# Kernel optimization log

Measured on AMD Instinct MI355X. Metric: run time of the kernel, lower is better.

## Reference

```python
import jax, jax.numpy as jnp
import numpy as np

N = 100000   # num variables
D_IN = 512
D_OUT = 512
C = 4096     # num clusters
K = 32       # vars per cluster
E = 16384    # cluster edges
S = 16       # shared vars per edge
H = 4        # num heads
NEG_SLOPE = 0.2


def setup_inputs() -> dict:
    key = jax.random.key(0)
    ks = jax.random.split(key, 8)
    xav = (6.0 / (D_IN + D_OUT)) ** 0.5  # xavier_uniform bound
    x_var = jax.random.normal(ks[0], (N, D_IN), dtype=jnp.float32)
    W_Q = jax.random.uniform(ks[1], (D_OUT, D_IN), jnp.float32, -xav, xav)
    W_K = jax.random.uniform(ks[2], (D_OUT, D_IN), jnp.float32, -xav, xav)
    W_V = jax.random.uniform(ks[3], (D_OUT, D_IN), jnp.float32, -xav, xav)
    head_weights = jnp.ones((H,), jnp.float32)
    cluster_var_ids = jax.random.randint(ks[4], (C, K), 0, N)
    cluster_edge_index = jax.random.randint(ks[5], (2, E), 0, C)
    shared_vars = jax.random.randint(ks[6], (E, S), 0, N)
    return {
        'x_var': x_var, 'W_Q': W_Q, 'W_K': W_K, 'W_V': W_V,
        'head_weights': head_weights,
        'cluster_var_ids': cluster_var_ids,
        'cluster_edge_index': cluster_edge_index,
        'shared_vars': shared_vars,
        'active_heads': 4,
    }


def reference(x_var, W_Q, W_K, W_V, head_weights,
              cluster_var_ids, cluster_edge_index, shared_vars, active_heads):
    # Per-cluster mean pooling over member variables: [C, D_in]
    cluster_feats = x_var[cluster_var_ids].mean(axis=1)
    # Linear projections (torch Linear: y = x @ W.T)
    Q = cluster_feats @ W_Q.T   # [C, D_out]
    Kc = cluster_feats @ W_K.T  # [C, D_out]
    V = cluster_feats @ W_V.T   # [C, D_out]
    c1 = cluster_edge_index[0]  # [E] source clusters
    c2 = cluster_edge_index[1]  # [E] target clusters
    # Scalar dot-product attention per cluster edge
    scale = jnp.asarray(D_OUT, jnp.float32) ** 0.5
    scores = jnp.einsum('ed,ed->e', Q[c1], Kc[c2]) / scale
    scores = jnp.where(scores >= 0, scores, NEG_SLOPE * scores)  # leaky_relu
    attn = jax.nn.sigmoid(scores) * head_weights[:active_heads].mean()  # [E]
    # Per-edge message = attn * V[c2], broadcast to each shared var of the edge
    upd = attn[:, None] * V[c2]                                   # [E, D_out]
    upd_flat = jnp.broadcast_to(upd[:, None, :], (E, S, D_OUT)).reshape(E * S, D_OUT)
    x_out = x_var.at[shared_vars.reshape(-1)].add(upd_flat)
    return x_out
```

## Files before the change

### kernel.cpp

```cpp
#include <hip/hip_runtime.h>
#include <hip/hip_bf16.h>
#include <math.h>

#define N_VARS    100000
#define D_DIM     512
#define C_CLUST   4096
#define K_VARS    32
#define E_EDGES   16384
#define S_SHARED  16
#define H_HEADS   4
#define CAP       32
#define NEG_SLOPE 0.2f

typedef __bf16 bf16x8_t __attribute__((ext_vector_type(8)));
typedef float  f32x4_t  __attribute__((ext_vector_type(4)));

__device__ __forceinline__ unsigned int f32_to_bf16_bits(float f) {
    unsigned int u = __builtin_bit_cast(unsigned int, f);
    unsigned int lsb = (u >> 16) & 1u;
    u += 0x7fffu + lsb;
    return u >> 16;
}
__device__ __forceinline__ unsigned int pack_bf16x2(float a, float b) {
    return (f32_to_bf16_bits(b) << 16) | f32_to_bf16_bits(a);
}

__device__ __forceinline__ int decode_active_heads(const int* p) {
    int raw = p[0];
    if (raw >= 1 && raw <= H_HEADS) return raw;
    float f = __builtin_bit_cast(float, raw);
    if (f >= 1.0f && f <= (float)H_HEADS) return (int)f;
    return H_HEADS;
}

__global__ void convert_w_kernel(const float* __restrict__ Wq,
                                 const float* __restrict__ Wk,
                                 const float* __restrict__ Wv,
                                 unsigned int* __restrict__ Wb) {
    const float* W = (blockIdx.y == 0) ? Wq : (blockIdx.y == 1) ? Wk : Wv;
    int i = blockIdx.x * blockDim.x + threadIdx.x;
    float2 w = ((const float2*)W)[i];
    Wb[(size_t)blockIdx.y * (D_DIM * D_DIM / 2) + i] = pack_bf16x2(w.x, w.y);
}

__global__ void pool_kernel(const float* __restrict__ x,
                            const int* __restrict__ cvid,
                            unsigned int* __restrict__ cfb ) {
    int c = blockIdx.x;
    int t = threadIdx.x;
    float a0 = 0.f, a1 = 0.f;
#pragma unroll 4
    for (int k = 0; k < K_VARS; ++k) {
        int v = cvid[c * K_VARS + k];
        float2 w = ((const float2*)(x + (size_t)v * D_DIM))[t];
        a0 += w.x;
        a1 += w.y;
    }
    const float inv = 1.0f / (float)K_VARS;
    cfb[(size_t)c * (D_DIM / 2) + t] = pack_bf16x2(a0 * inv, a1 * inv);
}

__global__ __launch_bounds__(256) void gemm_kernel(
        const unsigned short* __restrict__ cfb,
        const unsigned short* __restrict__ Wb,
        float* __restrict__ Qo, float* __restrict__ Ko, float* __restrict__ Vo) {
    const unsigned short* W = Wb + (size_t)blockIdx.z * D_DIM * D_DIM;
    float* O = (blockIdx.z == 0) ? Qo : (blockIdx.z == 1) ? Ko : Vo;

    int wave = threadIdx.x >> 6;
    int lane = threadIdx.x & 63;
    int m0 = blockIdx.x * 64 + wave * 16;
    int n0 = blockIdx.y * 16;
    int mr = m0 + (lane & 15);
    int nr = n0 + (lane & 15);
    int kb = (lane >> 4) * 8;

    f32x4_t acc = {0.f, 0.f, 0.f, 0.f};
    for (int k0 = 0; k0 < D_DIM; k0 += 32) {
        bf16x8_t a = *(const bf16x8_t*)(cfb + (size_t)mr * D_DIM + k0 + kb);
        bf16x8_t b = *(const bf16x8_t*)(W   + (size_t)nr * D_DIM + k0 + kb);
        acc = __builtin_amdgcn_mfma_f32_16x16x32_bf16(a, b, acc, 0, 0, 0);
    }
    int col = n0 + (lane & 15);
    int rb  = m0 + (lane >> 4) * 4;
#pragma unroll
    for (int r = 0; r < 4; ++r)
        O[(size_t)(rb + r) * D_DIM + col] = acc[r];
}

__global__ void score_kernel(const float* __restrict__ Q,
                             const float* __restrict__ Kc,
                             const int* __restrict__ cei,
                             const float* __restrict__ hw,
                             const int* __restrict__ active_heads,
                             float* __restrict__ attn) {
    int e = blockIdx.x * 4 + (threadIdx.x >> 6);
    int lane = threadIdx.x & 63;
    int c1 = cei[e];
    int c2 = cei[E_EDGES + e];
    const float* q = Q  + (size_t)c1 * D_DIM;
    const float* k = Kc + (size_t)c2 * D_DIM;
    float s = 0.f;
#pragma unroll
    for (int j = 0; j < 8; ++j)
        s += q[lane + 64 * j] * k[lane + 64 * j];
#pragma unroll
    for (int off = 32; off > 0; off >>= 1)
        s += __shfl_xor(s, off);
    if (lane == 0) {
        int ah = decode_active_heads(active_heads);
        float m = 0.f;
        for (int h = 0; h < ah; ++h) m += hw[h];
        m /= (float)ah;
        float sc = s * (1.0f / sqrtf((float)D_DIM));
        sc = sc >= 0.f ? sc : NEG_SLOPE * sc;
        attn[e] = m / (1.f + __expf(-sc));
    }
}

__global__ void fill_kernel(const int* __restrict__ shared_vars,
                            int* __restrict__ counts,
                            int* __restrict__ bucket) {
    int j = blockIdx.x * blockDim.x + threadIdx.x;
    if (j >= E_EDGES * S_SHARED) return;
    int v = shared_vars[j];
    int pos = atomicAdd(&counts[v], 1);
    if (pos < CAP) bucket[(size_t)v * CAP + pos] = j >> 4;
}

__global__ void gather_kernel(const float* __restrict__ x,
                              const float* __restrict__ V,
                              const float* __restrict__ attn,
                              const int* __restrict__ cei,
                              const int* __restrict__ counts,
                              const int* __restrict__ bucket,
                              float* __restrict__ out) {
    int v = blockIdx.x;
    int t = threadIdx.x;
    float2 xx = ((const float2*)(x + (size_t)v * D_DIM))[t];
    float a0 = xx.x, a1 = xx.y;
    int cnt = counts[v];
    if (cnt > CAP) cnt = CAP;
    for (int k = 0; k < cnt; ++k) {
        int e  = bucket[(size_t)v * CAP + k];
        int c2 = cei[E_EDGES + e];
        float a = attn[e];
        float2 vv = ((const float2*)(V + (size_t)c2 * D_DIM))[t];
        a0 += a * vv.x;
        a1 += a * vv.y;
    }
    float2 o; o.x = a0; o.y = a1;
    ((float2*)(out + (size_t)v * D_DIM))[t] = o;
}

extern "C" void kernel_launch(void* const* d_in, const int* in_sizes, int n_in,
                              void* d_out, int out_size, void* d_ws, size_t ws_size,
                              hipStream_t stream) {
    const float* x_var = (const float*)d_in[0];
    const float* W_Q   = (const float*)d_in[1];
    const float* W_K   = (const float*)d_in[2];
    const float* W_V   = (const float*)d_in[3];
    const float* hw    = (const float*)d_in[4];
    const int* cvid  = (const int*)d_in[5];
    const int* cei   = (const int*)d_in[6];
    const int* shv   = (const int*)d_in[7];
    const int* ahp   = (const int*)d_in[8];

    char* ws = (char*)d_ws;
    const size_t MiB = 1024 * 1024;
    unsigned int* cfb = (unsigned int*)(ws + 0);
    unsigned int* Wb  = (unsigned int*)(ws + 4  * MiB);
    float* Q    = (float*)(ws + 6  * MiB);
    float* Kc   = (float*)(ws + 14 * MiB);
    float* V    = (float*)(ws + 22 * MiB);
    float* attn = (float*)(ws + 30 * MiB);
    int* counts = (int*)(ws + 30 * MiB + 65536);
    int* bucket = (int*)(ws + 31 * MiB);

    convert_w_kernel<<<dim3(D_DIM * D_DIM / 2 / 256, 3), 256, 0, stream>>>(
        W_Q, W_K, W_V, Wb);

    pool_kernel<<<C_CLUST, 256, 0, stream>>>(x_var, cvid, cfb);

    gemm_kernel<<<dim3(C_CLUST / 64, D_DIM / 16, 3), 256, 0, stream>>>(
        (const unsigned short*)cfb, (const unsigned short*)Wb, Q, Kc, V);

    score_kernel<<<E_EDGES / 4, 256, 0, stream>>>(Q, Kc, cei, hw, ahp, attn);

    hipMemsetAsync(counts, 0, (size_t)N_VARS * sizeof(int), stream);
    fill_kernel<<<(E_EDGES * S_SHARED + 255) / 256, 256, 0, stream>>>(shv, counts, bucket);

    gather_kernel<<<N_VARS, 256, 0, stream>>>(x_var, V, attn, cei, counts, bucket,
                                              (float*)d_out);
}
```

Baseline: 586.0 us.

## Vectorize pool/score/gather, widen GEMM tile, pack attn and cluster into bucket

Pool and gather now run two rows per block and use float4 loads. The GEMM computes four 16x16 MFMA tiles per wave so each A fragment is reused across 64 output columns. Score uses float4 loads. The fill kernel packs a bf16 attention weight and the target cluster id into one bucket word, which removes the dependent cei and attn lookups in gather. Storing attention in bf16 costs precision, and the cluster id is masked to 12 bits, which assumes C is at most 4096.

```diff
diff --git a/kernel.cpp b/kernel.cpp
--- a/kernel.cpp
+++ b/kernel.cpp
@@ -24,6 +24,10 @@
 __device__ __forceinline__ unsigned int pack_bf16x2(float a, float b) {
     return (f32_to_bf16_bits(b) << 16) | f32_to_bf16_bits(a);
 }
+__device__ __forceinline__ float bf16_bits_to_f32(unsigned int h) {
+    unsigned int u = h << 16;
+    return __builtin_bit_cast(float, u);
+}
 
 __device__ __forceinline__ int decode_active_heads(const int* p) {
     int raw = p[0];
@@ -45,19 +49,21 @@
 
 __global__ void pool_kernel(const float* __restrict__ x,
                             const int* __restrict__ cvid,
-                            unsigned int* __restrict__ cfb ) {
-    int c = blockIdx.x;
-    int t = threadIdx.x;
-    float a0 = 0.f, a1 = 0.f;
+                            uint2* __restrict__ cfb ) {
+    int c = blockIdx.x * 2 + (threadIdx.x >> 7);
+    int t = threadIdx.x & 127;
+    float4 acc = {0.f, 0.f, 0.f, 0.f};
 #pragma unroll 4
     for (int k = 0; k < K_VARS; ++k) {
         int v = cvid[c * K_VARS + k];
-        float2 w = ((const float2*)(x + (size_t)v * D_DIM))[t];
-        a0 += w.x;
-        a1 += w.y;
+        float4 w = ((const float4*)(x + (size_t)v * D_DIM))[t];
+        acc.x += w.x; acc.y += w.y; acc.z += w.z; acc.w += w.w;
     }
     const float inv = 1.0f / (float)K_VARS;
-    cfb[(size_t)c * (D_DIM / 2) + t] = pack_bf16x2(a0 * inv, a1 * inv);
+    uint2 o;
+    o.x = pack_bf16x2(acc.x * inv, acc.y * inv);
+    o.y = pack_bf16x2(acc.z * inv, acc.w * inv);
+    cfb[(size_t)c * (D_DIM / 4) + t] = o;
 }
 
 __global__ __launch_bounds__(256) void gemm_kernel(
@@ -70,22 +76,39 @@
     int wave = threadIdx.x >> 6;
     int lane = threadIdx.x & 63;
     int m0 = blockIdx.x * 64 + wave * 16;
-    int n0 = blockIdx.y * 16;
+    int n0 = blockIdx.y * 64;
     int mr = m0 + (lane & 15);
-    int nr = n0 + (lane & 15);
     int kb = (lane >> 4) * 8;
 
-    f32x4_t acc = {0.f, 0.f, 0.f, 0.f};
+    f32x4_t acc0 = {0.f,0.f,0.f,0.f}, acc1 = {0.f,0.f,0.f,0.f};
+    f32x4_t acc2 = {0.f,0.f,0.f,0.f}, acc3 = {0.f,0.f,0.f,0.f};
+    const unsigned short* arow = cfb + (size_t)mr * D_DIM + kb;
+    const unsigned short* b0r  = W + (size_t)(n0 +  0 + (lane & 15)) * D_DIM + kb;
+    const unsigned short* b1r  = W + (size_t)(n0 + 16 + (lane & 15)) * D_DIM + kb;
+    const unsigned short* b2r  = W + (size_t)(n0 + 32 + (lane & 15)) * D_DIM + kb;
+    const unsigned short* b3r  = W + (size_t)(n0 + 48 + (lane & 15)) * D_DIM + kb;
+#pragma unroll 4
     for (int k0 = 0; k0 < D_DIM; k0 += 32) {
-        bf16x8_t a = *(const bf16x8_t*)(cfb + (size_t)mr * D_DIM + k0 + kb);
-        bf16x8_t b = *(const bf16x8_t*)(W   + (size_t)nr * D_DIM + k0 + kb);
-        acc = __builtin_amdgcn_mfma_f32_16x16x32_bf16(a, b, acc, 0, 0, 0);
-    }
-    int col = n0 + (lane & 15);
-    int rb  = m0 + (lane >> 4) * 4;
+        bf16x8_t a  = *(const bf16x8_t*)(arow + k0);
+        bf16x8_t b0 = *(const bf16x8_t*)(b0r + k0);
+        bf16x8_t b1 = *(const bf16x8_t*)(b1r + k0);
+        bf16x8_t b2 = *(const bf16x8_t*)(b2r + k0);
+        bf16x8_t b3 = *(const bf16x8_t*)(b3r + k0);
+        acc0 = __builtin_amdgcn_mfma_f32_16x16x32_bf16(a, b0, acc0, 0, 0, 0);
+        acc1 = __builtin_amdgcn_mfma_f32_16x16x32_bf16(a, b1, acc1, 0, 0, 0);
+        acc2 = __builtin_amdgcn_mfma_f32_16x16x32_bf16(a, b2, acc2, 0, 0, 0);
+        acc3 = __builtin_amdgcn_mfma_f32_16x16x32_bf16(a, b3, acc3, 0, 0, 0);
+    }
+    int rb = m0 + (lane >> 4) * 4;
+    int cl = lane & 15;
 #pragma unroll
-    for (int r = 0; r < 4; ++r)
-        O[(size_t)(rb + r) * D_DIM + col] = acc[r];
+    for (int r = 0; r < 4; ++r) {
+        float* orow = O + (size_t)(rb + r) * D_DIM + n0 + cl;
+        orow[ 0] = acc0[r];
+        orow[16] = acc1[r];
+        orow[32] = acc2[r];
+        orow[48] = acc3[r];
+    }
 }
 
 __global__ void score_kernel(const float* __restrict__ Q,
@@ -98,12 +121,12 @@
     int lane = threadIdx.x & 63;
     int c1 = cei[e];
     int c2 = cei[E_EDGES + e];
-    const float* q = Q  + (size_t)c1 * D_DIM;
-    const float* k = Kc + (size_t)c2 * D_DIM;
-    float s = 0.f;
-#pragma unroll
-    for (int j = 0; j < 8; ++j)
-        s += q[lane + 64 * j] * k[lane + 64 * j];
+    const float4* q = (const float4*)(Q  + (size_t)c1 * D_DIM);
+    const float4* k = (const float4*)(Kc + (size_t)c2 * D_DIM);
+    float4 qa = q[lane], qb = q[lane + 64];
+    float4 ka = k[lane], kb = k[lane + 64];
+    float s = qa.x*ka.x + qa.y*ka.y + qa.z*ka.z + qa.w*ka.w
+            + qb.x*kb.x + qb.y*kb.y + qb.z*kb.z + qb.w*kb.w;
 #pragma unroll
     for (int off = 32; off > 0; off >>= 1)
         s += __shfl_xor(s, off);
@@ -119,38 +142,40 @@
 }
 
 __global__ void fill_kernel(const int* __restrict__ shared_vars,
+                            const int* __restrict__ cei,
+                            const float* __restrict__ attn,
                             int* __restrict__ counts,
-                            int* __restrict__ bucket) {
+                            unsigned int* __restrict__ bucket) {
     int j = blockIdx.x * blockDim.x + threadIdx.x;
     if (j >= E_EDGES * S_SHARED) return;
     int v = shared_vars[j];
+    int e = j >> 4;
     int pos = atomicAdd(&counts[v], 1);
-    if (pos < CAP) bucket[(size_t)v * CAP + pos] = j >> 4;
+    if (pos < CAP) {
+        unsigned int packed = (f32_to_bf16_bits(attn[e]) << 16) | (unsigned int)cei[E_EDGES + e];
+        bucket[(size_t)v * CAP + pos] = packed;
+    }
 }
 
 __global__ void gather_kernel(const float* __restrict__ x,
                               const float* __restrict__ V,
-                              const float* __restrict__ attn,
-                              const int* __restrict__ cei,
                               const int* __restrict__ counts,
-                              const int* __restrict__ bucket,
+                              const unsigned int* __restrict__ bucket,
                               float* __restrict__ out) {
-    int v = blockIdx.x;
-    int t = threadIdx.x;
-    float2 xx = ((const float2*)(x + (size_t)v * D_DIM))[t];
-    float a0 = xx.x, a1 = xx.y;
+    int v = blockIdx.x * 2 + (threadIdx.x >> 7);
+    int t = threadIdx.x & 127;
+    float4 a = ((const float4*)(x + (size_t)v * D_DIM))[t];
     int cnt = counts[v];
     if (cnt > CAP) cnt = CAP;
+    const unsigned int* bk = bucket + (size_t)v * CAP;
     for (int k = 0; k < cnt; ++k) {
-        int e  = bucket[(size_t)v * CAP + k];
-        int c2 = cei[E_EDGES + e];
-        float a = attn[e];
-        float2 vv = ((const float2*)(V + (size_t)c2 * D_DIM))[t];
-        a0 += a * vv.x;
-        a1 += a * vv.y;
-    }
-    float2 o; o.x = a0; o.y = a1;
-    ((float2*)(out + (size_t)v * D_DIM))[t] = o;
+        unsigned int pw = bk[k];
+        float at = bf16_bits_to_f32(pw >> 16);
+        int c2 = pw & 0xFFFu;
+        float4 vv = ((const float4*)(V + (size_t)c2 * D_DIM))[t];
+        a.x += at * vv.x; a.y += at * vv.y; a.z += at * vv.z; a.w += at * vv.w;
+    }
+    ((float4*)(out + (size_t)v * D_DIM))[t] = a;
 }
 
 extern "C" void kernel_launch(void* const* d_in, const int* in_sizes, int n_in,
@@ -175,21 +200,22 @@
     float* V    = (float*)(ws + 22 * MiB);
     float* attn = (float*)(ws + 30 * MiB);
     int* counts = (int*)(ws + 30 * MiB + 65536);
-    int* bucket = (int*)(ws + 31 * MiB);
+    unsigned int* bucket = (unsigned int*)(ws + 31 * MiB);
 
     convert_w_kernel<<<dim3(D_DIM * D_DIM / 2 / 256, 3), 256, 0, stream>>>(
         W_Q, W_K, W_V, Wb);
 
-    pool_kernel<<<C_CLUST, 256, 0, stream>>>(x_var, cvid, cfb);
-
-    gemm_kernel<<<dim3(C_CLUST / 64, D_DIM / 16, 3), 256, 0, stream>>>(
+    pool_kernel<<<C_CLUST / 2, 256, 0, stream>>>(x_var, cvid, (uint2*)cfb);
+
+    gemm_kernel<<<dim3(C_CLUST / 64, D_DIM / 64, 3), 256, 0, stream>>>(
         (const unsigned short*)cfb, (const unsigned short*)Wb, Q, Kc, V);
 
     score_kernel<<<E_EDGES / 4, 256, 0, stream>>>(Q, Kc, cei, hw, ahp, attn);
 
     hipMemsetAsync(counts, 0, (size_t)N_VARS * sizeof(int), stream);
-    fill_kernel<<<(E_EDGES * S_SHARED + 255) / 256, 256, 0, stream>>>(shv, counts, bucket);
-
-    gather_kernel<<<N_VARS, 256, 0, stream>>>(x_var, V, attn, cei, counts, bucket,
-                                              (float*)d_out);
-}
+    fill_kernel<<<(E_EDGES * S_SHARED + 255) / 256, 256, 0, stream>>>(
+        shv, cei, attn, counts, bucket);
+
+    gather_kernel<<<N_VARS / 2, 256, 0, stream>>>(x_var, V, counts, bucket,
+                                                  (float*)d_out);
+}
```

Result: faster. 531.2 us (-9.4%).
